# Kernel optimization log

Hardware: AMD Instinct MI355X
Metric: run time of the kernel (lower is better)

## Reference

```python
import jax, jax.numpy as jnp
import numpy as np

B, C, H, W = 64, 2048, 14, 14
D, S, ITERS, EPS, HID = 256, 8, 3, 1e-8, 512


def build_pos(h, w, d):
    gy, gx = np.meshgrid(np.arange(h), np.arange(w), indexing='ij')
    q = d // 4
    omega = 1.0 / (10000.0 ** (np.arange(q) / q))
    ey = gy.reshape(-1, 1) * omega
    ex = gx.reshape(-1, 1) * omega
    pe = np.concatenate([np.sin(ey), np.cos(ey), np.sin(ex), np.cos(ex)], axis=1)
    return jnp.asarray(pe[None], jnp.float32)  # (1, h*w, d)


def layernorm(x, g, b, eps=1e-5):
    m = x.mean(-1, keepdims=True)
    v = ((x - m) ** 2).mean(-1, keepdims=True)
    return (x - m) * jax.lax.rsqrt(v + eps) * g + b


def setup_inputs() -> dict:
    key = jax.random.key(0)
    ks = jax.random.split(key, 16)
    w = lambda k, shp, s=0.02: jax.random.normal(k, shp, jnp.float32) * s
    inp = {
        'x': jax.random.normal(ks[0], (B, C, H, W), jnp.float32),
        'slot_noise': jax.random.normal(ks[1], (B, S, D), jnp.float32),
        'conv_w': w(ks[2], (C, D)), 'conv_b': jnp.zeros((D,), jnp.float32),
        'pos': build_pos(H, W, D),
        'slots_mu': jax.random.normal(ks[3], (1, 1, D), jnp.float32),
        'slots_logsigma': -jnp.ones((1, 1, D), jnp.float32),
        'qw': w(ks[4], (D, D)), 'qb': jnp.zeros((D,), jnp.float32),
        'kw': w(ks[5], (D, D)), 'kb': jnp.zeros((D,), jnp.float32),
        'vw': w(ks[6], (D, D)), 'vb': jnp.zeros((D,), jnp.float32),
        'gru_wih': w(ks[7], (D, 3 * D)), 'gru_whh': w(ks[8], (D, 3 * D)),
        'gru_bih': jnp.zeros((3 * D,), jnp.float32), 'gru_bhh': jnp.zeros((3 * D,), jnp.float32),
        'w1': w(ks[9], (D, HID)), 'b1': jnp.zeros((HID,), jnp.float32),
        'w2': w(ks[10], (HID, D)), 'b2': jnp.zeros((D,), jnp.float32),
        'ln_in_g': jnp.ones((D,), jnp.float32), 'ln_in_b': jnp.zeros((D,), jnp.float32),
        'ln_s_g': jnp.ones((D,), jnp.float32), 'ln_s_b': jnp.zeros((D,), jnp.float32),
        'ln_ff_g': jnp.ones((D,), jnp.float32), 'ln_ff_b': jnp.zeros((D,), jnp.float32),
    }
    return inp


def reference(x, slot_noise, conv_w, conv_b, pos, slots_mu, slots_logsigma,
              qw, qb, kw, kb, vw, vb, gru_wih, gru_whh, gru_bih, gru_bhh,
              w1, b1, w2, b2, ln_in_g, ln_in_b, ln_s_g, ln_s_b, ln_ff_g, ln_ff_b):
    b, c, h, w_ = x.shape
    d = qw.shape[0]
    scale = d ** (-0.5)
    # (B,C,H,W) -> (B,N,C) -> project -> add pos
    xt = x.transpose(0, 2, 3, 1).reshape(b, h * w_, c)
    xt = xt @ conv_w + conv_b + pos
    # slot init
    slots = slots_mu + jnp.exp(slots_logsigma) * slot_noise  # (B,S,D)
    inp = layernorm(xt, ln_in_g, ln_in_b)
    k = inp @ kw + kb
    v = inp @ vw + vb
    attn = None
    for _ in range(ITERS):
        slots_prev = slots
        s = layernorm(slots, ln_s_g, ln_s_b)
        q = s @ qw + qb
        dots = jnp.einsum('bid,bjd->bij', q, k) * scale  # (B,S,N)
        attn = jax.nn.softmax(dots, axis=1) + EPS  # softmax over slots
        attn = attn / attn.sum(-1, keepdims=True)  # renormalize over keys
        updates = jnp.einsum('bjd,bij->bid', v, attn)  # (B,S,D)
        # GRUCell (torch semantics)
        gi = updates @ gru_wih + gru_bih
        gh = slots_prev @ gru_whh + gru_bhh
        ir, iz, inn = jnp.split(gi, 3, axis=-1)
        hr, hz, hn = jnp.split(gh, 3, axis=-1)
        r = jax.nn.sigmoid(ir + hr)
        z = jax.nn.sigmoid(iz + hz)
        nn_ = jnp.tanh(inn + r * hn)
        slots = (1.0 - z) * nn_ + z * slots_prev
        ff = layernorm(slots, ln_ff_g, ln_ff_b)
        slots = slots + (jax.nn.relu(ff @ w1 + b1)) @ w2 + b2
    attn_map = attn.reshape(b, S, h, w_)
    return slots, attn_map
```

## Files before the change

kernel.cpp:

```cpp
#include <hip/hip_runtime.h>
#include <stdint.h>

#define HWN 196
#define CIN 2048
#define DD  256
#define BB  64
#define NSLOT 8
#define KVPAD 224
#define MTOT 12544
#define BKP 128

typedef __attribute__((ext_vector_type(8))) short short8;
typedef __attribute__((ext_vector_type(4))) float f32x4;
typedef __attribute__((ext_vector_type(4))) unsigned short us4;

__device__ __forceinline__ ushort f2bf(float f){ union{float f;uint32_t u;}v;v.f=f;uint32_t u=v.u;return (ushort)((u+0x7FFFu+((u>>16)&1u))>>16);}
__device__ __forceinline__ float bf2f(ushort h){ union{uint32_t u;float f;}v;v.u=((uint32_t)h)<<16;return v.f;}
__device__ __forceinline__ float sigm(float x){ return 1.f/(1.f+expf(-x)); }

__device__ __forceinline__ short8 ldsY(const ushort* buf, int LD, int kt, int lane){
    int row = lane & 15;
    int ch = kt*4 + (lane>>4);
    return *(const short8*)&buf[row*LD + ((ch ^ (row&7))<<3)];
}
__device__ __forceinline__ short8 gX(const ushort* base, int K, int nrow, int kt, int lane){
    return *(const short8*)&base[(size_t)nrow*K + kt*32 + (lane>>4)*8];
}

struct TD { const float* s; ushort* d; int R, C, t0; };
struct TD8 { TD a[8]; };

__global__ __launch_bounds__(256) void k_prep(TD8 td){
    __shared__ float tile[32][33];
    int bt = blockIdx.x;
    int mi = 0;
    #pragma unroll
    for (int i = 1; i < 8; ++i) if (bt >= td.a[i].t0) mi = i;
    TD d = td.a[mi];
    int lt = bt - d.t0;
    int tilesx = (d.C + 31) >> 5;
    int cb = (lt % tilesx) * 32, rb = (lt / tilesx) * 32;
    int tx = threadIdx.x & 31, ty = threadIdx.x >> 5;
    for (int i = ty; i < 32; i += 8) {
        int r = rb + i, c = cb + tx;
        tile[i][tx] = (r < d.R && c < d.C) ? d.s[(size_t)r * d.C + c] : 0.f;
    }
    __syncthreads();
    for (int i = ty; i < 32; i += 8) {
        int c = cb + i, r = rb + tx;
        if (c < d.C && r < d.R) d.d[(size_t)c * d.R + r] = f2bf(tile[tx][i]);
    }
}

__global__ __launch_bounds__(512) void k_proj(const float* __restrict__ x,
        const ushort* __restrict__ cwT, float* __restrict__ Cpart,
        int SK, int ksteps){
    __shared__ ushort As[2][64*BKP];
    const int t = threadIdx.x, lane = t & 63, wv = t >> 6;
    const int tile = blockIdx.x / SK, kq = blockIdx.x % SK;
    const int bm = tile * 64;
    const int kbase = kq * (ksteps * BKP);

    const int am = t & 63, kg = t >> 6;
    const int mg = bm + am;
    const int ab = mg / HWN, ap = mg % HWN;
    const float* aptr = x + (size_t)ab*(CIN*HWN) + ap + (size_t)kbase*HWN;

    f32x4 acc[4][2] = {};
    float areg[16];

    #pragma unroll
    for (int j = 0; j < 16; ++j) areg[j] = aptr[(size_t)(kg*16+j)*HWN];
    {
        short8 av0, av1;
        #pragma unroll
        for (int j = 0; j < 8; ++j){ av0[j] = (short)f2bf(areg[j]); av1[j] = (short)f2bf(areg[8+j]); }
        int ch0 = kg*2;
        *(short8*)&As[0][am*BKP + ((ch0^(am&7))<<3)] = av0;
        *(short8*)&As[0][am*BKP + (((ch0+1)^(am&7))<<3)] = av1;
    }
    __syncthreads();
    int cur = 0;
    for (int kt = 0; kt < ksteps; ++kt){
        if (kt < ksteps-1){
            #pragma unroll
            for (int j = 0; j < 16; ++j)
                areg[j] = aptr[(size_t)((kt+1)*BKP + kg*16+j)*HWN];
        }
        short8 bfr[4][2];
        #pragma unroll
        for (int kk = 0; kk < 4; ++kk)
            #pragma unroll
            for (int ni = 0; ni < 2; ++ni){
                int n = wv*32 + ni*16 + (lane&15);
                bfr[kk][ni] = *(const short8*)&cwT[(size_t)n*CIN + kbase + kt*BKP + kk*32 + (lane>>4)*8];
            }
        #pragma unroll
        for (int kk = 0; kk < 4; ++kk){
            short8 afr[4];
            #pragma unroll
            for (int mi = 0; mi < 4; ++mi){
                int row = mi*16 + (lane&15);
                int ch = kk*4 + (lane>>4);
                afr[mi] = *(const short8*)&As[cur][row*BKP + ((ch^(row&7))<<3)];
            }
            #pragma unroll
            for (int mi = 0; mi < 4; ++mi)
                #pragma unroll
                for (int ni = 0; ni < 2; ++ni)
                    acc[mi][ni] = __builtin_amdgcn_mfma_f32_16x16x32_bf16(afr[mi], bfr[kk][ni], acc[mi][ni], 0,0,0);
        }
        if (kt < ksteps-1){
            short8 av0, av1;
            #pragma unroll
            for (int j = 0; j < 8; ++j){ av0[j] = (short)f2bf(areg[j]); av1[j] = (short)f2bf(areg[8+j]); }
            int ch0 = kg*2;
            *(short8*)&As[cur^1][am*BKP + ((ch0^(am&7))<<3)] = av0;
            *(short8*)&As[cur^1][am*BKP + (((ch0+1)^(am&7))<<3)] = av1;
        }
        __syncthreads();
        cur ^= 1;
    }
    float* outp = Cpart + (size_t)kq*MTOT*DD;
    #pragma unroll
    for (int mi = 0; mi < 4; ++mi){
        #pragma unroll
        for (int ni = 0; ni < 2; ++ni){
            int n = wv*32 + ni*16 + (lane&15);
            #pragma unroll
            for (int r = 0; r < 4; ++r){
                int m = bm + mi*16 + (lane>>4)*4 + r;
                outp[(size_t)m*DD + n] = acc[mi][ni][r];
            }
        }
    }
}

__global__ __launch_bounds__(512) void k_red(const float* __restrict__ Cpart, int SK,
        const float* __restrict__ cb, const float* __restrict__ pos,
        const float* __restrict__ lng, const float* __restrict__ lnb,
        const ushort* __restrict__ kwT, const ushort* __restrict__ vwT,
        const float* __restrict__ kb, const float* __restrict__ vb,
        ushort* __restrict__ kbf, ushort* __restrict__ vT){
    __shared__ ushort As[32*256];
    const int t = threadIdx.x, lane = t & 63, wv = t >> 6;
    const int b = blockIdx.x / 7, pblk = blockIdx.x % 7;
    {
        int row = t >> 4, seg = t & 15;
        int pin = pblk*32 + row;
        int grow = b*HWN + pin;
        if (grow > MTOT-1) grow = MTOT-1;
        int p = pin < HWN ? pin : HWN-1;
        const float* pp = pos + (size_t)p*DD + seg*16;
        float f[16];
        #pragma unroll
        for (int q = 0; q < 4; ++q){
            f32x4 pv = *(const f32x4*)&pp[q*4];
            f32x4 cv = *(const f32x4*)&cb[seg*16 + q*4];
            #pragma unroll
            for (int r2 = 0; r2 < 4; ++r2) f[q*4+r2] = pv[r2] + cv[r2];
        }
        for (int sk = 0; sk < SK; ++sk){
            const float* cp = Cpart + (size_t)sk*MTOT*DD + (size_t)grow*DD + seg*16;
            #pragma unroll
            for (int q = 0; q < 4; ++q){
                f32x4 a = *(const f32x4*)&cp[q*4];
                #pragma unroll
                for (int r2 = 0; r2 < 4; ++r2) f[q*4+r2] += a[r2];
            }
        }
        float s = 0.f, sq = 0.f;
        #pragma unroll
        for (int j = 0; j < 16; ++j){ s += f[j]; sq += f[j]*f[j]; }
        #pragma unroll
        for (int m = 8; m >= 1; m >>= 1){ s += __shfl_xor(s, m, 64); sq += __shfl_xor(sq, m, 64); }
        float mean = s * (1.f/256.f);
        float rs = rsqrtf(sq*(1.f/256.f) - mean*mean + 1e-5f);
        int d0 = seg*16;
        short8 o0, o1;
        #pragma unroll
        for (int j = 0; j < 8; ++j){
            o0[j] = (short)f2bf((f[j]   - mean)*rs*lng[d0+j]   + lnb[d0+j]);
            o1[j] = (short)f2bf((f[8+j] - mean)*rs*lng[d0+8+j] + lnb[d0+8+j]);
        }
        int ch0 = seg*2;
        *(short8*)&As[row*256 + ((ch0^(row&7))<<3)] = o0;
        *(short8*)&As[row*256 + (((ch0+1)^(row&7))<<3)] = o1;
    }
    __syncthreads();
    f32x4 acck[2][2] = {}, accv[2][2] = {};
    const int n0 = wv*32;
    #pragma unroll
    for (int kt = 0; kt < 8; ++kt){
        short8 afr[2];
        #pragma unroll
        for (int mi = 0; mi < 2; ++mi){
            int row = mi*16 + (lane&15);
            int ch = kt*4 + (lane>>4);
            afr[mi] = *(const short8*)&As[row*256 + ((ch^(row&7))<<3)];
        }
        #pragma unroll
        for (int ni = 0; ni < 2; ++ni){
            int n = n0 + ni*16 + (lane&15);
            int koff = kt*32 + (lane>>4)*8;
            short8 bk = *(const short8*)&kwT[(size_t)n*DD + koff];
            short8 bv = *(const short8*)&vwT[(size_t)n*DD + koff];
            #pragma unroll
            for (int mi = 0; mi < 2; ++mi){
                acck[mi][ni] = __builtin_amdgcn_mfma_f32_16x16x32_bf16(afr[mi], bk, acck[mi][ni],0,0,0);
                accv[mi][ni] = __builtin_amdgcn_mfma_f32_16x16x32_bf16(afr[mi], bv, accv[mi][ni],0,0,0);
            }
        }
    }
    #pragma unroll
    for (int mi = 0; mi < 2; ++mi){
        #pragma unroll
        for (int ni = 0; ni < 2; ++ni){
            int n = n0 + ni*16 + (lane&15);
            float kbn = kb[n], vbn = vb[n];
            int pl0 = pblk*32 + mi*16 + (lane>>4)*4;
            us4 pk;
            #pragma unroll
            for (int r = 0; r < 4; ++r){
                kbf[((size_t)b*KVPAD + pl0 + r)*DD + n] = f2bf(acck[mi][ni][r] + kbn);
                pk[r] = f2bf(accv[mi][ni][r] + vbn);
            }
            *(us4*)&vT[((size_t)b*DD + n)*KVPAD + pl0] = pk;
        }
    }
}

__global__ __launch_bounds__(512) void k_init(const float* __restrict__ noise,
        const float* __restrict__ mu, const float* __restrict__ lsig,
        const ushort* __restrict__ qwT, const float* __restrict__ qb,
        const float* __restrict__ gs, const float* __restrict__ bs,
        float* __restrict__ slots, ushort* __restrict__ qbuf){
    __shared__ float Sld[16*256];
    __shared__ ushort Ysn[16*256];
    __shared__ float part[8][16][2];
    __shared__ float stats[16][2];
    const int t = threadIdx.x, lane = t & 63, w = t >> 6;
    const int bb = blockIdx.x, rbase = bb*16;
    {
        int row = t>>5, ch = t&31; int d = ch*8;
        f32x4 n0 = *(const f32x4*)&noise[(size_t)(rbase+row)*DD + d];
        f32x4 n1 = *(const f32x4*)&noise[(size_t)(rbase+row)*DD + d + 4];
        f32x4 m0 = *(const f32x4*)&mu[d];
        f32x4 m1 = *(const f32x4*)&mu[d+4];
        f32x4 l0 = *(const f32x4*)&lsig[d];
        f32x4 l1 = *(const f32x4*)&lsig[d+4];
        f32x4 s0, s1;
        #pragma unroll
        for (int j = 0; j < 4; ++j){
            s0[j] = m0[j] + expf(l0[j])*n0[j];
            s1[j] = m1[j] + expf(l1[j])*n1[j];
        }
        *(f32x4*)&slots[(size_t)(rbase+row)*DD + d] = s0;
        *(f32x4*)&slots[(size_t)(rbase+row)*DD + d + 4] = s1;
        *(f32x4*)&Sld[row*256 + d] = s0;
        *(f32x4*)&Sld[row*256 + d + 4] = s1;
    }
    __syncthreads();
    f32x4 sv[2];
    #pragma unroll
    for (int sub = 0; sub < 2; ++sub){
        int d0 = w*32 + sub*16 + (lane>>4)*4;
        sv[sub] = *(const f32x4*)&Sld[(lane&15)*256 + d0];
    }
    {
        float lsum = 0.f, lsq = 0.f;
        #pragma unroll
        for (int sub = 0; sub < 2; ++sub)
            #pragma unroll
            for (int r = 0; r < 4; ++r){ float v = sv[sub][r]; lsum += v; lsq += v*v; }
        lsum += __shfl_xor(lsum, 16, 64); lsum += __shfl_xor(lsum, 32, 64);
        lsq  += __shfl_xor(lsq, 16, 64);  lsq  += __shfl_xor(lsq, 32, 64);
        if (lane < 16){ part[w][lane][0] = lsum; part[w][lane][1] = lsq; }
    }
    __syncthreads();
    if (t < 16){
        float a = 0.f, c = 0.f;
        #pragma unroll
        for (int i = 0; i < 8; ++i){ a += part[i][t][0]; c += part[i][t][1]; }
        float mean = a*(1.f/256.f);
        stats[t][0] = mean;
        stats[t][1] = rsqrtf(c*(1.f/256.f) - mean*mean + 1e-5f);
    }
    __syncthreads();
    {
        int slot = lane&15;
        float mean = stats[slot][0], rs = stats[slot][1];
        #pragma unroll
        for (int sub = 0; sub < 2; ++sub){
            int d0 = w*32 + sub*16 + (lane>>4)*4;
            f32x4 g4 = *(const f32x4*)&gs[d0];
            f32x4 b4 = *(const f32x4*)&bs[d0];
            us4 o;
            #pragma unroll
            for (int r = 0; r < 4; ++r) o[r] = f2bf((sv[sub][r]-mean)*rs*g4[r] + b4[r]);
            int ch = d0>>3;
            *(us4*)&Ysn[slot*256 + ((ch^(slot&7))<<3) + (d0&7)] = o;
        }
    }
    __syncthreads();
    f32x4 qa[2] = {};
    #pragma unroll
    for (int kt = 0; kt < 8; ++kt){
        short8 ysn = ldsY(Ysn, 256, kt, lane);
        #pragma unroll
        for (int sub = 0; sub < 2; ++sub){
            int nrow = w*32 + sub*16 + (lane&15);
            short8 xx = gX(qwT, 256, nrow, kt, lane);
            qa[sub] = __builtin_amdgcn_mfma_f32_16x16x32_bf16(xx, ysn, qa[sub], 0,0,0);
        }
    }
    #pragma unroll
    for (int sub = 0; sub < 2; ++sub){
        int qd0 = w*32 + sub*16 + (lane>>4)*4;
        f32x4 qb4 = *(const f32x4*)&qb[qd0];
        us4 o;
        #pragma unroll
        for (int r = 0; r < 4; ++r) o[r] = f2bf((qa[sub][r]+qb4[r])*0.0625f);
        *(us4*)&qbuf[(size_t)(rbase+(lane&15))*DD + qd0] = o;
    }
}

__device__ __forceinline__ float sm_ep(f32x4 acc, int f, int lane, ushort* Xat, int srow){
    int k0 = f*16 + (lane>>4)*4;
    us4 o;
    float ps = 0.f;
    #pragma unroll
    for (int r = 0; r < 4; ++r){
        float v = acc[r];
        float mx = v;
        mx = fmaxf(mx, __shfl_xor(mx, 1, 64));
        mx = fmaxf(mx, __shfl_xor(mx, 2, 64));
        mx = fmaxf(mx, __shfl_xor(mx, 4, 64));
        float e = expf(v - mx);
        float se = e;
        se += __shfl_xor(se, 1, 64);
        se += __shfl_xor(se, 2, 64);
        se += __shfl_xor(se, 4, 64);
        float val = e/se + 1e-8f;
        if (k0 + r >= HWN) val = 0.f;
        ps += val;
        o[r] = f2bf(val);
    }
    int ch = k0 >> 3;
    *(us4*)&Xat[srow*256 + ((ch^(srow&7))<<3) + (k0&7)] = o;
    return ps;
}

__global__ __launch_bounds__(1024, 4) void k_slot(
        const ushort* __restrict__ qbuf, const ushort* __restrict__ kbf,
        const ushort* __restrict__ vT, float* __restrict__ slots,
        ushort* __restrict__ qout,
        const ushort* __restrict__ wihT, const ushort* __restrict__ whhT,
        const float* __restrict__ bih, const float* __restrict__ bhh,
        const ushort* __restrict__ w1T, const float* __restrict__ b1,
        const ushort* __restrict__ w2T, const float* __restrict__ b2,
        const float* __restrict__ gff, const float* __restrict__ bff,
        const float* __restrict__ gs, const float* __restrict__ bs,
        const ushort* __restrict__ qwT, const float* __restrict__ qb,
        float* __restrict__ out_slots, float* __restrict__ out_attn,
        int final_){
    __shared__ ushort Yq[16*256];
    __shared__ ushort Xat[16*256];
    __shared__ ushort Yupd[16*256];
    __shared__ ushort Yslb[16*256];
    __shared__ ushort Ysn[16*256];
    __shared__ ushort Yh[16*512];
    __shared__ float wpart[16][16];
    __shared__ float invk[16];
    __shared__ float part[16][16][2];
    __shared__ float stats[16][2];
    const int t = threadIdx.x, lane = t & 63, w = t >> 6;
    const int b = blockIdx.x;
    const int rbase = b * NSLOT;
    const int srow = lane & 15;
    const int srd = (srow < NSLOT) ? srow : 0;

    if (t < 256){
        int row = t>>5, ch = t&31;
        short8 v = *(const short8*)&qbuf[(size_t)(rbase+row)*DD + ch*8];
        *(short8*)&Yq[row*256 + ((ch^(row&7))<<3)] = v;
        f32x4 s0 = *(const f32x4*)&slots[(size_t)(rbase+row)*DD + ch*8];
        f32x4 s1 = *(const f32x4*)&slots[(size_t)(rbase+row)*DD + ch*8 + 4];
        short8 sv;
        #pragma unroll
        for (int j = 0; j < 4; ++j){ sv[j] = (short)f2bf(s0[j]); sv[4+j] = (short)f2bf(s1[j]); }
        *(short8*)&Yslb[row*256 + ((ch^(row&7))<<3)] = sv;
    } else if (t < 512){
        int i = t - 256;
        int row = (i>>5) + 8, ch = i&31;
        short8 z;
        #pragma unroll
        for (int j = 0; j < 8; ++j) z[j] = 0;
        *(short8*)&Yq[row*256 + ((ch^(row&7))<<3)] = z;
        *(short8*)&Yupd[row*256 + ((ch^(row&7))<<3)] = z;
        *(short8*)&Yslb[row*256 + ((ch^(row&7))<<3)] = z;
    }
    __syncthreads();
    if (w < 14){
        short8 yf[8];
        #pragma unroll
        for (int kt = 0; kt < 8; ++kt) yf[kt] = ldsY(Yq, 256, kt, lane);
        const ushort* kb_ = kbf + (size_t)b*KVPAD*DD;
        const int r0 = w*16 + (lane&15);
        short8 xa[2];
        xa[0] = gX(kb_, 256, r0, 0, lane);
        f32x4 accA = {};
        #pragma unroll
        for (int kt = 0; kt < 8; ++kt){
            int cu = kt & 1, nx = cu ^ 1;
            if (kt < 7) xa[nx] = gX(kb_, 256, r0, kt+1, lane);
            accA = __builtin_amdgcn_mfma_f32_16x16x32_bf16(xa[cu], yf[kt], accA, 0,0,0);
        }
        float ps = sm_ep(accA, w, lane, Xat, srow);
        ps += __shfl_xor(ps, 16, 64);
        ps += __shfl_xor(ps, 32, 64);
        if (lane < 16) wpart[w][lane] = ps;
    } else {
        if (lane < 16) wpart[w][lane] = 0.f;
    }
    __syncthreads();
    if (t < 16){
        float s = 0.f;
        #pragma unroll
        for (int i = 0; i < 16; ++i) s += wpart[i][t];
        invk[t] = 1.f/s;
    }
    f32x4 pv;
    {
        short8 xat[7];
        #pragma unroll
        for (int kt = 0; kt < 7; ++kt) xat[kt] = ldsY(Xat, 256, kt, lane);
        const ushort* vb_ = vT + (size_t)b*DD*KVPAD;
        const int d0r = w*16 + (lane&15);
        short8 ya[2];
        ya[0] = gX(vb_, KVPAD, d0r, 0, lane);
        f32x4 aA = {};
        #pragma unroll
        for (int kt = 0; kt < 7; ++kt){
            int cu = kt & 1, nx = cu ^ 1;
            if (kt < 6) ya[nx] = gX(vb_, KVPAD, d0r, kt+1, lane);
            aA = __builtin_amdgcn_mfma_f32_16x16x32_bf16(xat[kt], ya[cu], aA, 0,0,0);
        }
        pv = aA;
    }
    __syncthreads();
    {
        f32x4 iv = *(const f32x4*)&invk[(lane>>4)*4];
        int d0 = w*16;
        #pragma unroll
        for (int r = 0; r < 4; ++r){
            int s2 = (lane>>4)*4 + r;
            if (s2 < NSLOT){
                int d = d0 + (lane&15);
                int ch = d >> 3;
                Yupd[s2*256 + ((ch^(s2&7))<<3) + (d&7)] = f2bf(pv[r]*iv[r]);
            }
        }
    }
    if (final_){
        for (int idx = t; idx < NSLOT*HWN; idx += 1024){
            int slot = idx/HWN, key = idx - slot*HWN;
            int ch = key >> 3;
            out_attn[(size_t)b*NSLOT*HWN + idx] =
                bf2f(Xat[slot*256 + ((ch^(slot&7))<<3) + (key&7)]) * invk[slot];
        }
    }
    __syncthreads();
    f32x4 gi[3] = {}, gh[3] = {};
    {
        int nrw[3];
        #pragma unroll
        for (int g = 0; g < 3; ++g) nrw[g] = g*256 + w*16 + (lane&15);
        short8 xw[2][6];
        #pragma unroll
        for (int g = 0; g < 3; ++g){
            xw[0][g]   = gX(wihT, 256, nrw[g], 0, lane);
            xw[0][3+g] = gX(whhT, 256, nrw[g], 0, lane);
        }
        #pragma unroll
        for (int kt = 0; kt < 8; ++kt){
            int cu = kt & 1, nx = cu ^ 1;
            if (kt < 7){
                #pragma unroll
                for (int g = 0; g < 3; ++g){
                    xw[nx][g]   = gX(wihT, 256, nrw[g], kt+1, lane);
                    xw[nx][3+g] = gX(whhT, 256, nrw[g], kt+1, lane);
                }
            }
            short8 yu = ldsY(Yupd, 256, kt, lane);
            short8 ys = ldsY(Yslb, 256, kt, lane);
            #pragma unroll
            for (int g = 0; g < 3; ++g){
                gi[g] = __builtin_amdgcn_mfma_f32_16x16x32_bf16(xw[cu][g],   yu, gi[g], 0,0,0);
                gh[g] = __builtin_amdgcn_mfma_f32_16x16x32_bf16(xw[cu][3+g], ys, gh[g], 0,0,0);
            }
        }
    }
    f32x4 snew;
    {
        int d0 = w*16 + (lane>>4)*4;
        f32x4 sp  = *(const f32x4*)&slots[(size_t)(rbase + srd)*DD + d0];
        f32x4 bir = *(const f32x4*)&bih[d0];
        f32x4 biz = *(const f32x4*)&bih[256 + d0];
        f32x4 bin = *(const f32x4*)&bih[512 + d0];
        f32x4 bhr = *(const f32x4*)&bhh[d0];
        f32x4 bhz = *(const f32x4*)&bhh[256 + d0];
        f32x4 bhn = *(const f32x4*)&bhh[512 + d0];
        #pragma unroll
        for (int r = 0; r < 4; ++r){
            float ir = gi[0][r] + bir[r];
            float iz = gi[1][r] + biz[r];
            float in_ = gi[2][r] + bin[r];
            float hr = gh[0][r] + bhr[r];
            float hz = gh[1][r] + bhz[r];
            float hn = gh[2][r] + bhn[r];
            float rr = sigm(ir + hr);
            float zz = sigm(iz + hz);
            float nn = tanhf(in_ + rr*hn);
            snew[r] = (1.f - zz)*nn + zz*sp[r];
        }
    }
    {
        float lsum = 0.f, lsq = 0.f;
        #pragma unroll
        for (int r = 0; r < 4; ++r){ float v = snew[r]; lsum += v; lsq += v*v; }
        lsum += __shfl_xor(lsum, 16, 64); lsum += __shfl_xor(lsum, 32, 64);
        lsq  += __shfl_xor(lsq, 16, 64);  lsq  += __shfl_xor(lsq, 32, 64);
        if (lane < 16){ part[w][lane][0] = lsum; part[w][lane][1] = lsq; }
    }
    __syncthreads();
    if (t < 16){
        float a = 0.f, c = 0.f;
        #pragma unroll
        for (int i = 0; i < 16; ++i){ a += part[i][t][0]; c += part[i][t][1]; }
        float mean = a*(1.f/256.f);
        stats[t][0] = mean;
        stats[t][1] = rsqrtf(c*(1.f/256.f) - mean*mean + 1e-5f);
    }
    __syncthreads();
    {
        float mean = stats[srow][0], rs = stats[srow][1];
        int d0 = w*16 + (lane>>4)*4;
        f32x4 g4 = *(const f32x4*)&gff[d0];
        f32x4 b4 = *(const f32x4*)&bff[d0];
        us4 o;
        #pragma unroll
        for (int r = 0; r < 4; ++r) o[r] = f2bf((snew[r]-mean)*rs*g4[r] + b4[r]);
        int ch = d0 >> 3;
        *(us4*)&Ysn[srow*256 + ((ch^(srow&7))<<3) + (d0&7)] = o;
    }
    __syncthreads();
    {
        int nr1[2];
        #pragma unroll
        for (int s2 = 0; s2 < 2; ++s2) nr1[s2] = w*32 + s2*16 + (lane&15);
        short8 xw1[2][2];
        #pragma unroll
        for (int s2 = 0; s2 < 2; ++s2) xw1[0][s2] = gX(w1T, 256, nr1[s2], 0, lane);
        f32x4 hh[2] = {};
        #pragma unroll
        for (int kt = 0; kt < 8; ++kt){
            int cu = kt & 1, nx = cu ^ 1;
            if (kt < 7){
                #pragma unroll
                for (int s2 = 0; s2 < 2; ++s2) xw1[nx][s2] = gX(w1T, 256, nr1[s2], kt+1, lane);
            }
            short8 ysn = ldsY(Ysn, 256, kt, lane);
            #pragma unroll
            for (int s2 = 0; s2 < 2; ++s2)
                hh[s2] = __builtin_amdgcn_mfma_f32_16x16x32_bf16(xw1[cu][s2], ysn, hh[s2], 0,0,0);
        }
        #pragma unroll
        for (int s2 = 0; s2 < 2; ++s2){
            int n0 = w*32 + s2*16 + (lane>>4)*4;
            f32x4 b14 = *(const f32x4*)&b1[n0];
            us4 o;
            #pragma unroll
            for (int r = 0; r < 4; ++r) o[r] = f2bf(fmaxf(hh[s2][r] + b14[r], 0.f));
            int ch = n0 >> 3;
            *(us4*)&Yh[srow*512 + ((ch^(srow&7))<<3) + (n0&7)] = o;
        }
    }
    __syncthreads();
    f32x4 ns;
    {
        int nr2 = w*16 + (lane&15);
        short8 xw2[2];
        xw2[0] = gX(w2T, 512, nr2, 0, lane);
        f32x4 o2 = {};
        #pragma unroll
        for (int kt = 0; kt < 16; ++kt){
            int cu = kt & 1, nx = cu ^ 1;
            if (kt < 15) xw2[nx] = gX(w2T, 512, nr2, kt+1, lane);
            short8 yh = ldsY(Yh, 512, kt, lane);
            o2 = __builtin_amdgcn_mfma_f32_16x16x32_bf16(xw2[cu], yh, o2, 0,0,0);
        }
        float* dst = final_ ? out_slots : slots;
        int d0 = w*16 + (lane>>4)*4;
        f32x4 b24 = *(const f32x4*)&b2[d0];
        #pragma unroll
        for (int r = 0; r < 4; ++r) ns[r] = o2[r] + b24[r] + snew[r];
        if (srow < NSLOT)
            *(f32x4*)&dst[(size_t)(rbase + srow)*DD + d0] = ns;
    }
    if (final_) return;
    {
        float lsum = 0.f, lsq = 0.f;
        #pragma unroll
        for (int r = 0; r < 4; ++r){ float v = ns[r]; lsum += v; lsq += v*v; }
        lsum += __shfl_xor(lsum, 16, 64); lsum += __shfl_xor(lsum, 32, 64);
        lsq  += __shfl_xor(lsq, 16, 64);  lsq  += __shfl_xor(lsq, 32, 64);
        if (lane < 16){ part[w][lane][0] = lsum; part[w][lane][1] = lsq; }
    }
    __syncthreads();
    if (t < 16){
        float a = 0.f, c = 0.f;
        #pragma unroll
        for (int i = 0; i < 16; ++i){ a += part[i][t][0]; c += part[i][t][1]; }
        float mean = a*(1.f/256.f);
        stats[t][0] = mean;
        stats[t][1] = rsqrtf(c*(1.f/256.f) - mean*mean + 1e-5f);
    }
    __syncthreads();
    {
        float mean = stats[srow][0], rs = stats[srow][1];
        int d0 = w*16 + (lane>>4)*4;
        f32x4 g4 = *(const f32x4*)&gs[d0];
        f32x4 b4 = *(const f32x4*)&bs[d0];
        us4 o;
        #pragma unroll
        for (int r = 0; r < 4; ++r) o[r] = f2bf((ns[r]-mean)*rs*g4[r] + b4[r]);
        int ch = d0 >> 3;
        *(us4*)&Ysn[srow*256 + ((ch^(srow&7))<<3) + (d0&7)] = o;
    }
    __syncthreads();
    {
        int nrq = w*16 + (lane&15);
        short8 xq[2];
        xq[0] = gX(qwT, 256, nrq, 0, lane);
        f32x4 qa = {};
        #pragma unroll
        for (int kt = 0; kt < 8; ++kt){
            int cu = kt & 1, nx = cu ^ 1;
            if (kt < 7) xq[nx] = gX(qwT, 256, nrq, kt+1, lane);
            short8 ysn = ldsY(Ysn, 256, kt, lane);
            qa = __builtin_amdgcn_mfma_f32_16x16x32_bf16(xq[cu], ysn, qa, 0,0,0);
        }
        int qd0 = w*16 + (lane>>4)*4;
        f32x4 qb4 = *(const f32x4*)&qb[qd0];
        us4 o;
        #pragma unroll
        for (int r = 0; r < 4; ++r) o[r] = f2bf((qa[r]+qb4[r])*0.0625f);
        if (srow < NSLOT)
            *(us4*)&qout[(size_t)(rbase + srow)*DD + qd0] = o;
    }
}

extern "C" void kernel_launch(void* const* d_in, const int* in_sizes, int n_in,
                              void* d_out, int out_size, void* d_ws, size_t ws_size,
                              hipStream_t stream) {
    const float* x      = (const float*)d_in[0];
    const float* noise  = (const float*)d_in[1];
    const float* conv_w = (const float*)d_in[2];
    const float* conv_b = (const float*)d_in[3];
    const float* pos    = (const float*)d_in[4];
    const float* mu     = (const float*)d_in[5];
    const float* logsig = (const float*)d_in[6];
    const float* qw  = (const float*)d_in[7];
    const float* qb  = (const float*)d_in[8];
    const float* kw  = (const float*)d_in[9];
    const float* kb  = (const float*)d_in[10];
    const float* vw  = (const float*)d_in[11];
    const float* vb  = (const float*)d_in[12];
    const float* wih = (const float*)d_in[13];
    const float* whh = (const float*)d_in[14];
    const float* bih = (const float*)d_in[15];
    const float* bhh = (const float*)d_in[16];
    const float* w1  = (const float*)d_in[17];
    const float* b1  = (const float*)d_in[18];
    const float* w2  = (const float*)d_in[19];
    const float* b2  = (const float*)d_in[20];
    const float* g_in = (const float*)d_in[21];
    const float* b_in = (const float*)d_in[22];
    const float* g_s  = (const float*)d_in[23];
    const float* b_s  = (const float*)d_in[24];
    const float* g_ff = (const float*)d_in[25];
    const float* b_ff = (const float*)d_in[26];

    char* w = (char*)d_ws;
    ushort* kbf    = (ushort*)w; w += (size_t)BB*KVPAD*DD*2;
    ushort* vT     = (ushort*)w; w += (size_t)BB*DD*KVPAD*2;
    ushort* cwT    = (ushort*)w; w += (size_t)DD*CIN*2;
    ushort* qwT    = (ushort*)w; w += (size_t)DD*DD*2;
    ushort* kwT    = (ushort*)w; w += (size_t)DD*DD*2;
    ushort* vwT    = (ushort*)w; w += (size_t)DD*DD*2;
    ushort* wihT   = (ushort*)w; w += (size_t)768*DD*2;
    ushort* whhT   = (ushort*)w; w += (size_t)768*DD*2;
    ushort* w1T    = (ushort*)w; w += (size_t)512*DD*2;
    ushort* w2T    = (ushort*)w; w += (size_t)DD*512*2;
    ushort* qbb    = (ushort*)w; w += (size_t)BB*NSLOT*DD*2;
    float*  slotsb = (float*)w;  w += (size_t)BB*NSLOT*DD*4;
    float*  Cpart  = (float*)w;
    size_t fixedBytes = (size_t)(w - (char*)d_ws);
    int SK = (fixedBytes + (size_t)4*MTOT*DD*4 <= ws_size) ? 4 : 2;
    int ksteps = 16 / SK;

    float* out_slots = (float*)d_out;
    float* out_attn  = (float*)d_out + (size_t)BB*NSLOT*DD;

    TD8 td;
    td.a[0] = { conv_w, cwT, 2048, 256,    0 };
    td.a[1] = { qw,     qwT,  256, 256,  512 };
    td.a[2] = { kw,     kwT,  256, 256,  576 };
    td.a[3] = { vw,     vwT,  256, 256,  640 };
    td.a[4] = { wih,    wihT, 256, 768,  704 };
    td.a[5] = { whh,    whhT, 256, 768,  896 };
    td.a[6] = { w1,     w1T,  256, 512, 1088 };
    td.a[7] = { w2,     w2T,  512, 256, 1216 };

    k_prep<<<1344, 256, 0, stream>>>(td);
    k_proj<<<196*SK, 512, 0, stream>>>(x, cwT, Cpart, SK, ksteps);
    k_red<<<448, 512, 0, stream>>>(Cpart, SK, conv_b, pos, g_in, b_in,
                                   kwT, vwT, kb, vb, kbf, vT);
    k_init<<<32, 512, 0, stream>>>(noise, mu, logsig, qwT, qb, g_s, b_s, slotsb, qbb);
    for (int it = 0; it < 3; ++it){
        k_slot<<<BB, 1024, 0, stream>>>(qbb, kbf, vT, slotsb, qbb,
                                        wihT, whhT, bih, bhh, w1T, b1, w2T, b2,
                                        g_ff, b_ff, g_s, b_s, qwT, qb,
                                        out_slots, out_attn, it == 2);
    }
}
```

Measured before the change: 243.5 us.

## Fuse slot init and all three iterations into one persistent kernel, fix split-K at two

Measured after the change: 330.7 us. 1.36x slower.

```diff
diff --git a/kernel.cpp b/kernel.cpp
--- a/kernel.cpp
+++ b/kernel.cpp
@@ -53,13 +53,12 @@
 }
 
 __global__ __launch_bounds__(512) void k_proj(const float* __restrict__ x,
-        const ushort* __restrict__ cwT, float* __restrict__ Cpart,
-        int SK, int ksteps){
+        const ushort* __restrict__ cwT, float* __restrict__ Cpart){
     __shared__ ushort As[2][64*BKP];
     const int t = threadIdx.x, lane = t & 63, wv = t >> 6;
-    const int tile = blockIdx.x / SK, kq = blockIdx.x % SK;
+    const int tile = blockIdx.x >> 1, kq = blockIdx.x & 1;
     const int bm = tile * 64;
-    const int kbase = kq * (ksteps * BKP);
+    const int kbase = kq * 1024;
 
     const int am = t & 63, kg = t >> 6;
     const int mg = bm + am;
@@ -81,8 +80,8 @@
     }
     __syncthreads();
     int cur = 0;
-    for (int kt = 0; kt < ksteps; ++kt){
-        if (kt < ksteps-1){
+    for (int kt = 0; kt < 8; ++kt){
+        if (kt < 7){
             #pragma unroll
             for (int j = 0; j < 16; ++j)
                 areg[j] = aptr[(size_t)((kt+1)*BKP + kg*16+j)*HWN];
@@ -110,7 +109,7 @@
                 for (int ni = 0; ni < 2; ++ni)
                     acc[mi][ni] = __builtin_amdgcn_mfma_f32_16x16x32_bf16(afr[mi], bfr[kk][ni], acc[mi][ni], 0,0,0);
         }
-        if (kt < ksteps-1){
+        if (kt < 7){
             short8 av0, av1;
             #pragma unroll
             for (int j = 0; j < 8; ++j){ av0[j] = (short)f2bf(areg[j]); av1[j] = (short)f2bf(areg[8+j]); }
@@ -136,7 +135,7 @@
     }
 }
 
-__global__ __launch_bounds__(512) void k_red(const float* __restrict__ Cpart, int SK,
+__global__ __launch_bounds__(512) void k_red(const float* __restrict__ Cpart,
         const float* __restrict__ cb, const float* __restrict__ pos,
         const float* __restrict__ lng, const float* __restrict__ lnb,
         const ushort* __restrict__ kwT, const ushort* __restrict__ vwT,
@@ -151,27 +150,23 @@
         int grow = b*HWN + pin;
         if (grow > MTOT-1) grow = MTOT-1;
         int p = pin < HWN ? pin : HWN-1;
+        const float* c0 = Cpart + (size_t)grow*DD + seg*16;
+        const float* c1 = Cpart + (size_t)MTOT*DD + (size_t)grow*DD + seg*16;
         const float* pp = pos + (size_t)p*DD + seg*16;
         float f[16];
+        float s = 0.f, sq = 0.f;
         #pragma unroll
         for (int q = 0; q < 4; ++q){
+            f32x4 a  = *(const f32x4*)&c0[q*4];
+            f32x4 bq = *(const f32x4*)&c1[q*4];
             f32x4 pv = *(const f32x4*)&pp[q*4];
             f32x4 cv = *(const f32x4*)&cb[seg*16 + q*4];
             #pragma unroll
-            for (int r2 = 0; r2 < 4; ++r2) f[q*4+r2] = pv[r2] + cv[r2];
-        }
-        for (int sk = 0; sk < SK; ++sk){
-            const float* cp = Cpart + (size_t)sk*MTOT*DD + (size_t)grow*DD + seg*16;
-            #pragma unroll
-            for (int q = 0; q < 4; ++q){
-                f32x4 a = *(const f32x4*)&cp[q*4];
-                #pragma unroll
-                for (int r2 = 0; r2 < 4; ++r2) f[q*4+r2] += a[r2];
-            }
-        }
-        float s = 0.f, sq = 0.f;
-        #pragma unroll
-        for (int j = 0; j < 16; ++j){ s += f[j]; sq += f[j]*f[j]; }
+            for (int r2 = 0; r2 < 4; ++r2){
+                float v = a[r2] + bq[r2] + pv[r2] + cv[r2];
+                f[q*4+r2] = v; s += v; sq += v*v;
+            }
+        }
         #pragma unroll
         for (int m = 8; m >= 1; m >>= 1){ s += __shfl_xor(s, m, 64); sq += __shfl_xor(sq, m, 64); }
         float mean = s * (1.f/256.f);
@@ -227,101 +222,6 @@
             }
             *(us4*)&vT[((size_t)b*DD + n)*KVPAD + pl0] = pk;
         }
-    }
-}
-
-__global__ __launch_bounds__(512) void k_init(const float* __restrict__ noise,
-        const float* __restrict__ mu, const float* __restrict__ lsig,
-        const ushort* __restrict__ qwT, const float* __restrict__ qb,
-        const float* __restrict__ gs, const float* __restrict__ bs,
-        float* __restrict__ slots, ushort* __restrict__ qbuf){
-    __shared__ float Sld[16*256];
-    __shared__ ushort Ysn[16*256];
-    __shared__ float part[8][16][2];
-    __shared__ float stats[16][2];
-    const int t = threadIdx.x, lane = t & 63, w = t >> 6;
-    const int bb = blockIdx.x, rbase = bb*16;
-    {
-        int row = t>>5, ch = t&31; int d = ch*8;
-        f32x4 n0 = *(const f32x4*)&noise[(size_t)(rbase+row)*DD + d];
-        f32x4 n1 = *(const f32x4*)&noise[(size_t)(rbase+row)*DD + d + 4];
-        f32x4 m0 = *(const f32x4*)&mu[d];
-        f32x4 m1 = *(const f32x4*)&mu[d+4];
-        f32x4 l0 = *(const f32x4*)&lsig[d];
-        f32x4 l1 = *(const f32x4*)&lsig[d+4];
-        f32x4 s0, s1;
-        #pragma unroll
-        for (int j = 0; j < 4; ++j){
-            s0[j] = m0[j] + expf(l0[j])*n0[j];
-            s1[j] = m1[j] + expf(l1[j])*n1[j];
-        }
-        *(f32x4*)&slots[(size_t)(rbase+row)*DD + d] = s0;
-        *(f32x4*)&slots[(size_t)(rbase+row)*DD + d + 4] = s1;
-        *(f32x4*)&Sld[row*256 + d] = s0;
-        *(f32x4*)&Sld[row*256 + d + 4] = s1;
-    }
-    __syncthreads();
-    f32x4 sv[2];
-    #pragma unroll
-    for (int sub = 0; sub < 2; ++sub){
-        int d0 = w*32 + sub*16 + (lane>>4)*4;
-        sv[sub] = *(const f32x4*)&Sld[(lane&15)*256 + d0];
-    }
-    {
-        float lsum = 0.f, lsq = 0.f;
-        #pragma unroll
-        for (int sub = 0; sub < 2; ++sub)
-            #pragma unroll
-            for (int r = 0; r < 4; ++r){ float v = sv[sub][r]; lsum += v; lsq += v*v; }
-        lsum += __shfl_xor(lsum, 16, 64); lsum += __shfl_xor(lsum, 32, 64);
-        lsq  += __shfl_xor(lsq, 16, 64);  lsq  += __shfl_xor(lsq, 32, 64);
-        if (lane < 16){ part[w][lane][0] = lsum; part[w][lane][1] = lsq; }
-    }
-    __syncthreads();
-    if (t < 16){
-        float a = 0.f, c = 0.f;
-        #pragma unroll
-        for (int i = 0; i < 8; ++i){ a += part[i][t][0]; c += part[i][t][1]; }
-        float mean = a*(1.f/256.f);
-        stats[t][0] = mean;
-        stats[t][1] = rsqrtf(c*(1.f/256.f) - mean*mean + 1e-5f);
-    }
-    __syncthreads();
-    {
-        int slot = lane&15;
-        float mean = stats[slot][0], rs = stats[slot][1];
-        #pragma unroll
-        for (int sub = 0; sub < 2; ++sub){
-            int d0 = w*32 + sub*16 + (lane>>4)*4;
-            f32x4 g4 = *(const f32x4*)&gs[d0];
-            f32x4 b4 = *(const f32x4*)&bs[d0];
-            us4 o;
-            #pragma unroll
-            for (int r = 0; r < 4; ++r) o[r] = f2bf((sv[sub][r]-mean)*rs*g4[r] + b4[r]);
-            int ch = d0>>3;
-            *(us4*)&Ysn[slot*256 + ((ch^(slot&7))<<3) + (d0&7)] = o;
-        }
-    }
-    __syncthreads();
-    f32x4 qa[2] = {};
-    #pragma unroll
-    for (int kt = 0; kt < 8; ++kt){
-        short8 ysn = ldsY(Ysn, 256, kt, lane);
-        #pragma unroll
-        for (int sub = 0; sub < 2; ++sub){
-            int nrow = w*32 + sub*16 + (lane&15);
-            short8 xx = gX(qwT, 256, nrow, kt, lane);
-            qa[sub] = __builtin_amdgcn_mfma_f32_16x16x32_bf16(xx, ysn, qa[sub], 0,0,0);
-        }
-    }
-    #pragma unroll
-    for (int sub = 0; sub < 2; ++sub){
-        int qd0 = w*32 + sub*16 + (lane>>4)*4;
-        f32x4 qb4 = *(const f32x4*)&qb[qd0];
-        us4 o;
-        #pragma unroll
-        for (int r = 0; r < 4; ++r) o[r] = f2bf((qa[sub][r]+qb4[r])*0.0625f);
-        *(us4*)&qbuf[(size_t)(rbase+(lane&15))*DD + qd0] = o;
     }
 }
 
@@ -351,25 +251,25 @@
     return ps;
 }
 
-__global__ __launch_bounds__(1024, 4) void k_slot(
-        const ushort* __restrict__ qbuf, const ushort* __restrict__ kbf,
-        const ushort* __restrict__ vT, float* __restrict__ slots,
-        ushort* __restrict__ qout,
+__global__ __launch_bounds__(1024, 4) void k_slot3(
+        const float* __restrict__ noise, const float* __restrict__ mu,
+        const float* __restrict__ lsig,
+        const ushort* __restrict__ qwT, const float* __restrict__ qb,
+        const ushort* __restrict__ kbf, const ushort* __restrict__ vT,
         const ushort* __restrict__ wihT, const ushort* __restrict__ whhT,
         const float* __restrict__ bih, const float* __restrict__ bhh,
         const ushort* __restrict__ w1T, const float* __restrict__ b1,
         const ushort* __restrict__ w2T, const float* __restrict__ b2,
         const float* __restrict__ gff, const float* __restrict__ bff,
         const float* __restrict__ gs, const float* __restrict__ bs,
-        const ushort* __restrict__ qwT, const float* __restrict__ qb,
-        float* __restrict__ out_slots, float* __restrict__ out_attn,
-        int final_){
+        float* __restrict__ out_slots, float* __restrict__ out_attn){
     __shared__ ushort Yq[16*256];
     __shared__ ushort Xat[16*256];
     __shared__ ushort Yupd[16*256];
     __shared__ ushort Yslb[16*256];
     __shared__ ushort Ysn[16*256];
     __shared__ ushort Yh[16*512];
+    __shared__ float Sl[8*256];
     __shared__ float wpart[16][16];
     __shared__ float invk[16];
     __shared__ float part[16][16][2];
@@ -380,17 +280,7 @@
     const int srow = lane & 15;
     const int srd = (srow < NSLOT) ? srow : 0;
 
-    if (t < 256){
-        int row = t>>5, ch = t&31;
-        short8 v = *(const short8*)&qbuf[(size_t)(rbase+row)*DD + ch*8];
-        *(short8*)&Yq[row*256 + ((ch^(row&7))<<3)] = v;
-        f32x4 s0 = *(const f32x4*)&slots[(size_t)(rbase+row)*DD + ch*8];
-        f32x4 s1 = *(const f32x4*)&slots[(size_t)(rbase+row)*DD + ch*8 + 4];
-        short8 sv;
-        #pragma unroll
-        for (int j = 0; j < 4; ++j){ sv[j] = (short)f2bf(s0[j]); sv[4+j] = (short)f2bf(s1[j]); }
-        *(short8*)&Yslb[row*256 + ((ch^(row&7))<<3)] = sv;
-    } else if (t < 512){
+    if (t >= 256 && t < 512){
         int i = t - 256;
         int row = (i>>5) + 8, ch = i&31;
         short8 z;
@@ -400,264 +290,291 @@
         *(short8*)&Yupd[row*256 + ((ch^(row&7))<<3)] = z;
         *(short8*)&Yslb[row*256 + ((ch^(row&7))<<3)] = z;
     }
-    __syncthreads();
-    if (w < 14){
-        short8 yf[8];
-        #pragma unroll
-        for (int kt = 0; kt < 8; ++kt) yf[kt] = ldsY(Yq, 256, kt, lane);
-        const ushort* kb_ = kbf + (size_t)b*KVPAD*DD;
-        const int r0 = w*16 + (lane&15);
-        short8 xa[2];
-        xa[0] = gX(kb_, 256, r0, 0, lane);
-        f32x4 accA = {};
-        #pragma unroll
-        for (int kt = 0; kt < 8; ++kt){
-            int cu = kt & 1, nx = cu ^ 1;
-            if (kt < 7) xa[nx] = gX(kb_, 256, r0, kt+1, lane);
-            accA = __builtin_amdgcn_mfma_f32_16x16x32_bf16(xa[cu], yf[kt], accA, 0,0,0);
-        }
-        float ps = sm_ep(accA, w, lane, Xat, srow);
-        ps += __shfl_xor(ps, 16, 64);
-        ps += __shfl_xor(ps, 32, 64);
-        if (lane < 16) wpart[w][lane] = ps;
-    } else {
-        if (lane < 16) wpart[w][lane] = 0.f;
-    }
-    __syncthreads();
-    if (t < 16){
-        float s = 0.f;
-        #pragma unroll
-        for (int i = 0; i < 16; ++i) s += wpart[i][t];
-        invk[t] = 1.f/s;
-    }
-    f32x4 pv;
-    {
-        short8 xat[7];
-        #pragma unroll
-        for (int kt = 0; kt < 7; ++kt) xat[kt] = ldsY(Xat, 256, kt, lane);
-        const ushort* vb_ = vT + (size_t)b*DD*KVPAD;
-        const int d0r = w*16 + (lane&15);
-        short8 ya[2];
-        ya[0] = gX(vb_, KVPAD, d0r, 0, lane);
-        f32x4 aA = {};
-        #pragma unroll
-        for (int kt = 0; kt < 7; ++kt){
-            int cu = kt & 1, nx = cu ^ 1;
-            if (kt < 6) ya[nx] = gX(vb_, KVPAD, d0r, kt+1, lane);
-            aA = __builtin_amdgcn_mfma_f32_16x16x32_bf16(xat[kt], ya[cu], aA, 0,0,0);
-        }
-        pv = aA;
-    }
-    __syncthreads();
-    {
-        f32x4 iv = *(const f32x4*)&invk[(lane>>4)*4];
-        int d0 = w*16;
-        #pragma unroll
-        for (int r = 0; r < 4; ++r){
-            int s2 = (lane>>4)*4 + r;
-            if (s2 < NSLOT){
-                int d = d0 + (lane&15);
-                int ch = d >> 3;
-                Yupd[s2*256 + ((ch^(s2&7))<<3) + (d&7)] = f2bf(pv[r]*iv[r]);
-            }
-        }
-    }
-    if (final_){
-        for (int idx = t; idx < NSLOT*HWN; idx += 1024){
-            int slot = idx/HWN, key = idx - slot*HWN;
-            int ch = key >> 3;
-            out_attn[(size_t)b*NSLOT*HWN + idx] =
-                bf2f(Xat[slot*256 + ((ch^(slot&7))<<3) + (key&7)]) * invk[slot];
-        }
-    }
-    __syncthreads();
-    f32x4 gi[3] = {}, gh[3] = {};
-    {
-        int nrw[3];
-        #pragma unroll
-        for (int g = 0; g < 3; ++g) nrw[g] = g*256 + w*16 + (lane&15);
-        short8 xw[2][6];
-        #pragma unroll
-        for (int g = 0; g < 3; ++g){
-            xw[0][g]   = gX(wihT, 256, nrw[g], 0, lane);
-            xw[0][3+g] = gX(whhT, 256, nrw[g], 0, lane);
-        }
-        #pragma unroll
-        for (int kt = 0; kt < 8; ++kt){
-            int cu = kt & 1, nx = cu ^ 1;
-            if (kt < 7){
+    if (t < 512){
+        int idx = t*4;
+        int row = idx >> 8, d = idx & 255;
+        f32x4 nz = *(const f32x4*)&noise[((size_t)rbase+row)*DD + d];
+        f32x4 o;
+        #pragma unroll
+        for (int j = 0; j < 4; ++j) o[j] = mu[d+j] + expf(lsig[d+j])*nz[j];
+        *(f32x4*)&Sl[idx] = o;
+    }
+
+    for (int it = 0; it < 3; ++it){
+        __syncthreads();
+        if (t < 256){
+            int row = t>>5, ch = t&31;
+            f32x4 s0 = *(const f32x4*)&Sl[row*256 + ch*8];
+            f32x4 s1 = *(const f32x4*)&Sl[row*256 + ch*8 + 4];
+            short8 sv;
+            #pragma unroll
+            for (int j = 0; j < 4; ++j){ sv[j] = (short)f2bf(s0[j]); sv[4+j] = (short)f2bf(s1[j]); }
+            *(short8*)&Yslb[row*256 + ((ch^(row&7))<<3)] = sv;
+        }
+        f32x4 sv_;
+        {
+            int d0 = w*16 + (lane>>4)*4;
+            sv_ = *(const f32x4*)&Sl[srd*256 + d0];
+            float lsum = 0.f, lsq = 0.f;
+            #pragma unroll
+            for (int r = 0; r < 4; ++r){ float v = sv_[r]; lsum += v; lsq += v*v; }
+            lsum += __shfl_xor(lsum, 16, 64); lsum += __shfl_xor(lsum, 32, 64);
+            lsq  += __shfl_xor(lsq, 16, 64);  lsq  += __shfl_xor(lsq, 32, 64);
+            if (lane < 16){ part[w][lane][0] = lsum; part[w][lane][1] = lsq; }
+        }
+        __syncthreads();
+        if (t < 16){
+            float a = 0.f, c = 0.f;
+            #pragma unroll
+            for (int i = 0; i < 16; ++i){ a += part[i][t][0]; c += part[i][t][1]; }
+            float mean = a*(1.f/256.f);
+            stats[t][0] = mean;
+            stats[t][1] = rsqrtf(c*(1.f/256.f) - mean*mean + 1e-5f);
+        }
+        __syncthreads();
+        {
+            float mean = stats[srow][0], rs = stats[srow][1];
+            int d0 = w*16 + (lane>>4)*4;
+            f32x4 g4 = *(const f32x4*)&gs[d0];
+            f32x4 b4 = *(const f32x4*)&bs[d0];
+            us4 o;
+            #pragma unroll
+            for (int r = 0; r < 4; ++r) o[r] = f2bf((sv_[r]-mean)*rs*g4[r] + b4[r]);
+            int ch = d0 >> 3;
+            *(us4*)&Ysn[srow*256 + ((ch^(srow&7))<<3) + (d0&7)] = o;
+        }
+        __syncthreads();
+        {
+            int nrq = w*16 + (lane&15);
+            short8 xq[2];
+            xq[0] = gX(qwT, 256, nrq, 0, lane);
+            f32x4 qa = {};
+            #pragma unroll
+            for (int kt = 0; kt < 8; ++kt){
+                int cu = kt & 1, nx = cu ^ 1;
+                if (kt < 7) xq[nx] = gX(qwT, 256, nrq, kt+1, lane);
+                short8 ysn = ldsY(Ysn, 256, kt, lane);
+                qa = __builtin_amdgcn_mfma_f32_16x16x32_bf16(xq[cu], ysn, qa, 0,0,0);
+            }
+            int qd0 = w*16 + (lane>>4)*4;
+            f32x4 qb4 = *(const f32x4*)&qb[qd0];
+            us4 o;
+            #pragma unroll
+            for (int r = 0; r < 4; ++r) o[r] = f2bf((qa[r]+qb4[r])*0.0625f);
+            if (srow < NSLOT){
+                int ch = qd0 >> 3;
+                *(us4*)&Yq[srow*256 + ((ch^(srow&7))<<3) + (qd0&7)] = o;
+            }
+        }
+        __syncthreads();
+        if (w < 14){
+            short8 yf[8];
+            #pragma unroll
+            for (int kt = 0; kt < 8; ++kt) yf[kt] = ldsY(Yq, 256, kt, lane);
+            const ushort* kb_ = kbf + (size_t)b*KVPAD*DD;
+            const int r0 = w*16 + (lane&15);
+            short8 xa[2];
+            xa[0] = gX(kb_, 256, r0, 0, lane);
+            f32x4 accA = {};
+            #pragma unroll
+            for (int kt = 0; kt < 8; ++kt){
+                int cu = kt & 1, nx = cu ^ 1;
+                if (kt < 7) xa[nx] = gX(kb_, 256, r0, kt+1, lane);
+                accA = __builtin_amdgcn_mfma_f32_16x16x32_bf16(xa[cu], yf[kt], accA, 0,0,0);
+            }
+            float ps = sm_ep(accA, w, lane, Xat, srow);
+            ps += __shfl_xor(ps, 16, 64);
+            ps += __shfl_xor(ps, 32, 64);
+            if (lane < 16) wpart[w][lane] = ps;
+        } else {
+            if (lane < 16) wpart[w][lane] = 0.f;
+        }
+        __syncthreads();
+        if (t < 16){
+            float s = 0.f;
+            #pragma unroll
+            for (int i = 0; i < 16; ++i) s += wpart[i][t];
+            invk[t] = 1.f/s;
+        }
+        f32x4 pv;
+        {
+            short8 xat[7];
+            #pragma unroll
+            for (int kt = 0; kt < 7; ++kt) xat[kt] = ldsY(Xat, 256, kt, lane);
+            const ushort* vb_ = vT + (size_t)b*DD*KVPAD;
+            const int d0r = w*16 + (lane&15);
+            short8 ya[2];
+            ya[0] = gX(vb_, KVPAD, d0r, 0, lane);
+            f32x4 aA = {};
+            #pragma unroll
+            for (int kt = 0; kt < 7; ++kt){
+                int cu = kt & 1, nx = cu ^ 1;
+                if (kt < 6) ya[nx] = gX(vb_, KVPAD, d0r, kt+1, lane);
+                aA = __builtin_amdgcn_mfma_f32_16x16x32_bf16(xat[kt], ya[cu], aA, 0,0,0);
+            }
+            pv = aA;
+        }
+        __syncthreads();
+        {
+            f32x4 iv = *(const f32x4*)&invk[(lane>>4)*4];
+            int d0 = w*16;
+            #pragma unroll
+            for (int r = 0; r < 4; ++r){
+                int s2 = (lane>>4)*4 + r;
+                if (s2 < NSLOT){
+                    int d = d0 + (lane&15);
+                    int ch = d >> 3;
+                    Yupd[s2*256 + ((ch^(s2&7))<<3) + (d&7)] = f2bf(pv[r]*iv[r]);
+                }
+            }
+        }
+        if (it == 2){
+            for (int idx = t; idx < NSLOT*HWN; idx += 1024){
+                int slot = idx/HWN, key = idx - slot*HWN;
+                int ch = key >> 3;
+                out_attn[(size_t)b*NSLOT*HWN + idx] =
+                    bf2f(Xat[slot*256 + ((ch^(slot&7))<<3) + (key&7)]) * invk[slot];
+            }
+        }
+        __syncthreads();
+        f32x4 gi[3] = {}, gh[3] = {};
+        {
+            int nrw[3];
+            #pragma unroll
+            for (int g = 0; g < 3; ++g) nrw[g] = g*256 + w*16 + (lane&15);
+            short8 xw[2][6];
+            #pragma unroll
+            for (int g = 0; g < 3; ++g){
+                xw[0][g]   = gX(wihT, 256, nrw[g], 0, lane);
+                xw[0][3+g] = gX(whhT, 256, nrw[g], 0, lane);
+            }
+            #pragma unroll
+            for (int kt = 0; kt < 8; ++kt){
+                int cu = kt & 1, nx = cu ^ 1;
+                if (kt < 7){
+                    #pragma unroll
+                    for (int g = 0; g < 3; ++g){
+                        xw[nx][g]   = gX(wihT, 256, nrw[g], kt+1, lane);
+                        xw[nx][3+g] = gX(whhT, 256, nrw[g], kt+1, lane);
+                    }
+                }
+                short8 yu = ldsY(Yupd, 256, kt, lane);
+                short8 ys = ldsY(Yslb, 256, kt, lane);
                 #pragma unroll
                 for (int g = 0; g < 3; ++g){
-                    xw[nx][g]   = gX(wihT, 256, nrw[g], kt+1, lane);
-                    xw[nx][3+g] = gX(whhT, 256, nrw[g], kt+1, lane);
+                    gi[g] = __builtin_amdgcn_mfma_f32_16x16x32_bf16(xw[cu][g],   yu, gi[g], 0,0,0);
+                    gh[g] = __builtin_amdgcn_mfma_f32_16x16x32_bf16(xw[cu][3+g], ys, gh[g], 0,0,0);
                 }
             }
-            short8 yu = ldsY(Yupd, 256, kt, lane);
-            short8 ys = ldsY(Yslb, 256, kt, lane);
-            #pragma unroll
-            for (int g = 0; g < 3; ++g){
-                gi[g] = __builtin_amdgcn_mfma_f32_16x16x32_bf16(xw[cu][g],   yu, gi[g], 0,0,0);
-                gh[g] = __builtin_amdgcn_mfma_f32_16x16x32_bf16(xw[cu][3+g], ys, gh[g], 0,0,0);
-            }
-        }
-    }
-    f32x4 snew;
-    {
-        int d0 = w*16 + (lane>>4)*4;
-        f32x4 sp  = *(const f32x4*)&slots[(size_t)(rbase + srd)*DD + d0];
-        f32x4 bir = *(const f32x4*)&bih[d0];
-        f32x4 biz = *(const f32x4*)&bih[256 + d0];
-        f32x4 bin = *(const f32x4*)&bih[512 + d0];
-        f32x4 bhr = *(const f32x4*)&bhh[d0];
-        f32x4 bhz = *(const f32x4*)&bhh[256 + d0];
-        f32x4 bhn = *(const f32x4*)&bhh[512 + d0];
-        #pragma unroll
-        for (int r = 0; r < 4; ++r){
-            float ir = gi[0][r] + bir[r];
-            float iz = gi[1][r] + biz[r];
-            float in_ = gi[2][r] + bin[r];
-            float hr = gh[0][r] + bhr[r];
-            float hz = gh[1][r] + bhz[r];
-            float hn = gh[2][r] + bhn[r];
-            float rr = sigm(ir + hr);
-            float zz = sigm(iz + hz);
-            float nn = tanhf(in_ + rr*hn);
-            snew[r] = (1.f - zz)*nn + zz*sp[r];
-        }
-    }
-    {
-        float lsum = 0.f, lsq = 0.f;
-        #pragma unroll
-        for (int r = 0; r < 4; ++r){ float v = snew[r]; lsum += v; lsq += v*v; }
-        lsum += __shfl_xor(lsum, 16, 64); lsum += __shfl_xor(lsum, 32, 64);
-        lsq  += __shfl_xor(lsq, 16, 64);  lsq  += __shfl_xor(lsq, 32, 64);
-        if (lane < 16){ part[w][lane][0] = lsum; part[w][lane][1] = lsq; }
-    }
-    __syncthreads();
-    if (t < 16){
-        float a = 0.f, c = 0.f;
-        #pragma unroll
-        for (int i = 0; i < 16; ++i){ a += part[i][t][0]; c += part[i][t][1]; }
-        float mean = a*(1.f/256.f);
-        stats[t][0] = mean;
-        stats[t][1] = rsqrtf(c*(1.f/256.f) - mean*mean + 1e-5f);
-    }
-    __syncthreads();
-    {
-        float mean = stats[srow][0], rs = stats[srow][1];
-        int d0 = w*16 + (lane>>4)*4;
-        f32x4 g4 = *(const f32x4*)&gff[d0];
-        f32x4 b4 = *(const f32x4*)&bff[d0];
-        us4 o;
-        #pragma unroll
-        for (int r = 0; r < 4; ++r) o[r] = f2bf((snew[r]-mean)*rs*g4[r] + b4[r]);
-        int ch = d0 >> 3;
-        *(us4*)&Ysn[srow*256 + ((ch^(srow&7))<<3) + (d0&7)] = o;
-    }
-    __syncthreads();
-    {
-        int nr1[2];
-        #pragma unroll
-        for (int s2 = 0; s2 < 2; ++s2) nr1[s2] = w*32 + s2*16 + (lane&15);
-        short8 xw1[2][2];
-        #pragma unroll
-        for (int s2 = 0; s2 < 2; ++s2) xw1[0][s2] = gX(w1T, 256, nr1[s2], 0, lane);
-        f32x4 hh[2] = {};
-        #pragma unroll
-        for (int kt = 0; kt < 8; ++kt){
-            int cu = kt & 1, nx = cu ^ 1;
-            if (kt < 7){
+        }
+        f32x4 snew;
+        {
+            int d0 = w*16 + (lane>>4)*4;
+            f32x4 sp  = *(const f32x4*)&Sl[srd*256 + d0];
+            f32x4 bir = *(const f32x4*)&bih[d0];
+            f32x4 biz = *(const f32x4*)&bih[256 + d0];
+            f32x4 bin = *(const f32x4*)&bih[512 + d0];
+            f32x4 bhr = *(const f32x4*)&bhh[d0];
+            f32x4 bhz = *(const f32x4*)&bhh[256 + d0];
+            f32x4 bhn = *(const f32x4*)&bhh[512 + d0];
+            #pragma unroll
+            for (int r = 0; r < 4; ++r){
+                float ir = gi[0][r] + bir[r];
+                float iz = gi[1][r] + biz[r];
+                float in_ = gi[2][r] + bin[r];
+                float hr = gh[0][r] + bhr[r];
+                float hz = gh[1][r] + bhz[r];
+                float hn = gh[2][r] + bhn[r];
+                float rr = sigm(ir + hr);
+                float zz = sigm(iz + hz);
+                float nn = tanhf(in_ + rr*hn);
+                snew[r] = (1.f - zz)*nn + zz*sp[r];
+            }
+        }
+        {
+            float lsum = 0.f, lsq = 0.f;
+            #pragma unroll
+            for (int r = 0; r < 4; ++r){ float v = snew[r]; lsum += v; lsq += v*v; }
+            lsum += __shfl_xor(lsum, 16, 64); lsum += __shfl_xor(lsum, 32, 64);
+            lsq  += __shfl_xor(lsq, 16, 64);  lsq  += __shfl_xor(lsq, 32, 64);
+            if (lane < 16){ part[w][lane][0] = lsum; part[w][lane][1] = lsq; }
+        }
+        __syncthreads();
+        if (t < 16){
+            float a = 0.f, c = 0.f;
+            #pragma unroll
+            for (int i = 0; i < 16; ++i){ a += part[i][t][0]; c += part[i][t][1]; }
+            float mean = a*(1.f/256.f);
+            stats[t][0] = mean;
+            stats[t][1] = rsqrtf(c*(1.f/256.f) - mean*mean + 1e-5f);
+        }
+        __syncthreads();
+        {
+            float mean = stats[srow][0], rs = stats[srow][1];
+            int d0 = w*16 + (lane>>4)*4;
+            f32x4 g4 = *(const f32x4*)&gff[d0];
+            f32x4 b4 = *(const f32x4*)&bff[d0];
+            us4 o;
+            #pragma unroll
+            for (int r = 0; r < 4; ++r) o[r] = f2bf((snew[r]-mean)*rs*g4[r] + b4[r]);
+            int ch = d0 >> 3;
+            *(us4*)&Ysn[srow*256 + ((ch^(srow&7))<<3) + (d0&7)] = o;
+        }
+        __syncthreads();
+        {
+            int nr1[2];
+            #pragma unroll
+            for (int s2 = 0; s2 < 2; ++s2) nr1[s2] = w*32 + s2*16 + (lane&15);
+            short8 xw1[2][2];
+            #pragma unroll
+            for (int s2 = 0; s2 < 2; ++s2) xw1[0][s2] = gX(w1T, 256, nr1[s2], 0, lane);
+            f32x4 hh[2] = {};
+            #pragma unroll
+            for (int kt = 0; kt < 8; ++kt){
+                int cu = kt & 1, nx = cu ^ 1;
+                if (kt < 7){
+                    #pragma unroll
+                    for (int s2 = 0; s2 < 2; ++s2) xw1[nx][s2] = gX(w1T, 256, nr1[s2], kt+1, lane);
+                }
+                short8 ysn = ldsY(Ysn, 256, kt, lane);
                 #pragma unroll
-                for (int s2 = 0; s2 < 2; ++s2) xw1[nx][s2] = gX(w1T, 256, nr1[s2], kt+1, lane);
-            }
-            short8 ysn = ldsY(Ysn, 256, kt, lane);
-            #pragma unroll
-            for (int s2 = 0; s2 < 2; ++s2)
-                hh[s2] = __builtin_amdgcn_mfma_f32_16x16x32_bf16(xw1[cu][s2], ysn, hh[s2], 0,0,0);
-        }
-        #pragma unroll
-        for (int s2 = 0; s2 < 2; ++s2){
-            int n0 = w*32 + s2*16 + (lane>>4)*4;
-            f32x4 b14 = *(const f32x4*)&b1[n0];
-            us4 o;
-            #pragma unroll
-            for (int r = 0; r < 4; ++r) o[r] = f2bf(fmaxf(hh[s2][r] + b14[r], 0.f));
-            int ch = n0 >> 3;
-            *(us4*)&Yh[srow*512 + ((ch^(srow&7))<<3) + (n0&7)] = o;
-        }
-    }
-    __syncthreads();
-    f32x4 ns;
-    {
-        int nr2 = w*16 + (lane&15);
-        short8 xw2[2];
-        xw2[0] = gX(w2T, 512, nr2, 0, lane);
-        f32x4 o2 = {};
-        #pragma unroll
-        for (int kt = 0; kt < 16; ++kt){
-            int cu = kt & 1, nx = cu ^ 1;
-            if (kt < 15) xw2[nx] = gX(w2T, 512, nr2, kt+1, lane);
-            short8 yh = ldsY(Yh, 512, kt, lane);
-            o2 = __builtin_amdgcn_mfma_f32_16x16x32_bf16(xw2[cu], yh, o2, 0,0,0);
-        }
-        float* dst = final_ ? out_slots : slots;
-        int d0 = w*16 + (lane>>4)*4;
-        f32x4 b24 = *(const f32x4*)&b2[d0];
-        #pragma unroll
-        for (int r = 0; r < 4; ++r) ns[r] = o2[r] + b24[r] + snew[r];
-        if (srow < NSLOT)
-            *(f32x4*)&dst[(size_t)(rbase + srow)*DD + d0] = ns;
-    }
-    if (final_) return;
-    {
-        float lsum = 0.f, lsq = 0.f;
-        #pragma unroll
-        for (int r = 0; r < 4; ++r){ float v = ns[r]; lsum += v; lsq += v*v; }
-        lsum += __shfl_xor(lsum, 16, 64); lsum += __shfl_xor(lsum, 32, 64);
-        lsq  += __shfl_xor(lsq, 16, 64);  lsq  += __shfl_xor(lsq, 32, 64);
-        if (lane < 16){ part[w][lane][0] = lsum; part[w][lane][1] = lsq; }
-    }
-    __syncthreads();
-    if (t < 16){
-        float a = 0.f, c = 0.f;
-        #pragma unroll
-        for (int i = 0; i < 16; ++i){ a += part[i][t][0]; c += part[i][t][1]; }
-        float mean = a*(1.f/256.f);
-        stats[t][0] = mean;
-        stats[t][1] = rsqrtf(c*(1.f/256.f) - mean*mean + 1e-5f);
-    }
-    __syncthreads();
-    {
-        float mean = stats[srow][0], rs = stats[srow][1];
-        int d0 = w*16 + (lane>>4)*4;
-        f32x4 g4 = *(const f32x4*)&gs[d0];
-        f32x4 b4 = *(const f32x4*)&bs[d0];
-        us4 o;
-        #pragma unroll
-        for (int r = 0; r < 4; ++r) o[r] = f2bf((ns[r]-mean)*rs*g4[r] + b4[r]);
-        int ch = d0 >> 3;
-        *(us4*)&Ysn[srow*256 + ((ch^(srow&7))<<3) + (d0&7)] = o;
-    }
-    __syncthreads();
-    {
-        int nrq = w*16 + (lane&15);
-        short8 xq[2];
-        xq[0] = gX(qwT, 256, nrq, 0, lane);
-        f32x4 qa = {};
-        #pragma unroll
-        for (int kt = 0; kt < 8; ++kt){
-            int cu = kt & 1, nx = cu ^ 1;
-            if (kt < 7) xq[nx] = gX(qwT, 256, nrq, kt+1, lane);
-            short8 ysn = ldsY(Ysn, 256, kt, lane);
-            qa = __builtin_amdgcn_mfma_f32_16x16x32_bf16(xq[cu], ysn, qa, 0,0,0);
-        }
-        int qd0 = w*16 + (lane>>4)*4;
-        f32x4 qb4 = *(const f32x4*)&qb[qd0];
-        us4 o;
-        #pragma unroll
-        for (int r = 0; r < 4; ++r) o[r] = f2bf((qa[r]+qb4[r])*0.0625f);
-        if (srow < NSLOT)
-            *(us4*)&qout[(size_t)(rbase + srow)*DD + qd0] = o;
+                for (int s2 = 0; s2 < 2; ++s2)
+                    hh[s2] = __builtin_amdgcn_mfma_f32_16x16x32_bf16(xw1[cu][s2], ysn, hh[s2], 0,0,0);
+            }
+            #pragma unroll
+            for (int s2 = 0; s2 < 2; ++s2){
+                int n0 = w*32 + s2*16 + (lane>>4)*4;
+                f32x4 b14 = *(const f32x4*)&b1[n0];
+                us4 o;
+                #pragma unroll
+                for (int r = 0; r < 4; ++r) o[r] = f2bf(fmaxf(hh[s2][r] + b14[r], 0.f));
+                int ch = n0 >> 3;
+                *(us4*)&Yh[srow*512 + ((ch^(srow&7))<<3) + (n0&7)] = o;
+            }
+        }
+        __syncthreads();
+        {
+            int nr2 = w*16 + (lane&15);
+            short8 xw2[2];
+            xw2[0] = gX(w2T, 512, nr2, 0, lane);
+            f32x4 o2 = {};
+            #pragma unroll
+            for (int kt = 0; kt < 16; ++kt){
+                int cu = kt & 1, nx = cu ^ 1;
+                if (kt < 15) xw2[nx] = gX(w2T, 512, nr2, kt+1, lane);
+                short8 yh = ldsY(Yh, 512, kt, lane);
+                o2 = __builtin_amdgcn_mfma_f32_16x16x32_bf16(xw2[cu], yh, o2, 0,0,0);
+            }
+            int d0 = w*16 + (lane>>4)*4;
+            f32x4 b24 = *(const f32x4*)&b2[d0];
+            f32x4 ns;
+            #pragma unroll
+            for (int r = 0; r < 4; ++r) ns[r] = o2[r] + b24[r] + snew[r];
+            if (srow < NSLOT){
+                if (it == 2) *(f32x4*)&out_slots[((size_t)rbase + srow)*DD + d0] = ns;
+                else         *(f32x4*)&Sl[srow*256 + d0] = ns;
+            }
+        }
     }
 }
 
@@ -703,12 +620,7 @@
     ushort* whhT   = (ushort*)w; w += (size_t)768*DD*2;
     ushort* w1T    = (ushort*)w; w += (size_t)512*DD*2;
     ushort* w2T    = (ushort*)w; w += (size_t)DD*512*2;
-    ushort* qbb    = (ushort*)w; w += (size_t)BB*NSLOT*DD*2;
-    float*  slotsb = (float*)w;  w += (size_t)BB*NSLOT*DD*4;
-    float*  Cpart  = (float*)w;
-    size_t fixedBytes = (size_t)(w - (char*)d_ws);
-    int SK = (fixedBytes + (size_t)4*MTOT*DD*4 <= ws_size) ? 4 : 2;
-    int ksteps = 16 / SK;
+    float*  Cpart  = (float*)w;  w += (size_t)2*MTOT*DD*4;
 
     float* out_slots = (float*)d_out;
     float* out_attn  = (float*)d_out + (size_t)BB*NSLOT*DD;
@@ -724,14 +636,10 @@
     td.a[7] = { w2,     w2T,  512, 256, 1216 };
 
     k_prep<<<1344, 256, 0, stream>>>(td);
-    k_proj<<<196*SK, 512, 0, stream>>>(x, cwT, Cpart, SK, ksteps);
-    k_red<<<448, 512, 0, stream>>>(Cpart, SK, conv_b, pos, g_in, b_in,
+    k_proj<<<392, 512, 0, stream>>>(x, cwT, Cpart);
+    k_red<<<448, 512, 0, stream>>>(Cpart, conv_b, pos, g_in, b_in,
                                    kwT, vwT, kb, vb, kbf, vT);
-    k_init<<<32, 512, 0, stream>>>(noise, mu, logsig, qwT, qb, g_s, b_s, slotsb, qbb);
-    for (int it = 0; it < 3; ++it){
-        k_slot<<<BB, 1024, 0, stream>>>(qbb, kbf, vT, slotsb, qbb,
-                                        wihT, whhT, bih, bhh, w1T, b1, w2T, b2,
-                                        g_ff, b_ff, g_s, b_s, qwT, qb,
-                                        out_slots, out_attn, it == 2);
-    }
-}
+    k_slot3<<<BB, 1024, 0, stream>>>(noise, mu, logsig, qwT, qb, kbf, vT,
+                                     wihT, whhT, bih, bhh, w1T, b1, w2T, b2,
+                                     g_ff, b_ff, g_s, b_s, out_slots, out_attn);
+}
```
